# Kernel tuning notes

Hardware: AMD Instinct MI355X
Metric: run time of the kernel (lower is better)

The kernel has to match this reference:

```python
import jax, jax.numpy as jnp
import numpy as np

D_IN = 1024
D_OUT = 1024
NUM_HEADS = 16
HEAD_DIM = D_OUT // NUM_HEADS


def setup_inputs() -> dict:
    key = jax.random.key(0)
    ks = jax.random.split(key, 6)
    s = 0.02
    return {
        "x": jax.random.normal(ks[0], (4, 2048, D_IN), dtype=jnp.float32),
        "Wq": jax.random.normal(ks[1], (D_IN, D_OUT), dtype=jnp.float32) * s,
        "Wk": jax.random.normal(ks[2], (D_IN, D_OUT), dtype=jnp.float32) * s,
        "Wv": jax.random.normal(ks[3], (D_IN, D_OUT), dtype=jnp.float32) * s,
        "Wo": jax.random.normal(ks[4], (D_OUT, D_OUT), dtype=jnp.float32) * s,
        "bo": jax.random.normal(ks[5], (D_OUT,), dtype=jnp.float32) * s,
    }


def reference(x, Wq, Wk, Wv, Wo, bo):
    B, S, _ = x.shape
    # QKV projections (no bias), split into heads: [B, H, S, Dh]
    def split_heads(t):
        return t.reshape(B, S, NUM_HEADS, HEAD_DIM).transpose(0, 2, 1, 3)

    q = split_heads(x @ Wq)
    k = split_heads(x @ Wk)
    v = split_heads(x @ Wv)

    # causal scores [B, H, S, S]; note: original masks BEFORE scaling,
    # but -inf is scale-invariant so softmax(scores/sqrt(d)) with mask is identical.
    scores = jnp.einsum("bhqd,bhkd->bhqk", q, k) / jnp.sqrt(jnp.asarray(HEAD_DIM, x.dtype))
    causal = jnp.tril(jnp.ones((S, S), dtype=bool))
    scores = jnp.where(causal, scores, -jnp.inf)
    attn = jax.nn.softmax(scores, axis=-1)
    # dropout p=0.0 -> identity
    ctx = jnp.einsum("bhqk,bhkd->bhqd", attn, v)  # [B, H, S, Dh]
    ctx = ctx.transpose(0, 2, 1, 3).reshape(B, S, D_OUT)
    return ctx @ Wo + bo
```

## Files before the change

### kernel.cpp

```cpp
#include <hip/hip_runtime.h>
#include <hip/hip_bf16.h>
#include <math.h>


typedef __attribute__((ext_vector_type(8))) short short8;
typedef __attribute__((ext_vector_type(4))) float f32x4;

#define MFMA_BF16(a, b, c) __builtin_amdgcn_mfma_f32_16x16x32_bf16((a), (b), (c), 0, 0, 0)

__device__ __forceinline__ void gld_lds16(const void* g, void* l) {
  __builtin_amdgcn_global_load_lds((const __attribute__((address_space(1))) void*)g,
                                   (__attribute__((address_space(3))) void*)l, 16, 0, 0);
}

__global__ void prep_kernel(const float* __restrict__ x, __hip_bfloat16* __restrict__ xb,
                            const float* __restrict__ W0, const float* __restrict__ W1,
                            const float* __restrict__ W2, const float* __restrict__ W3,
                            __hip_bfloat16* __restrict__ T0, __hip_bfloat16* __restrict__ T1,
                            __hip_bfloat16* __restrict__ T2, __hip_bfloat16* __restrict__ T3) {
  const int bid = blockIdx.x, tid = threadIdx.x;
  if (bid < 8192) {
    int i = bid * 256 + tid;
    float4 v = ((const float4*)x)[i];
    __align__(8) __hip_bfloat16 tmp[4] = {__float2bfloat16(v.x), __float2bfloat16(v.y),
                                          __float2bfloat16(v.z), __float2bfloat16(v.w)};
    ((ushort4*)xb)[i] = *(const ushort4*)tmp;
  } else {
    int zz = bid - 8192;
    int z = zz >> 10, rem = zz & 1023;
    const float* W = (z == 0) ? W0 : (z == 1) ? W1 : (z == 2) ? W2 : W3;
    __hip_bfloat16* Wt = (z == 0) ? T0 : (z == 1) ? T1 : (z == 2) ? T2 : T3;
    __shared__ float tile[32][33];
    int tx = tid & 31, ty = tid >> 5;
    int n0 = (rem & 31) * 32, k0 = (rem >> 5) * 32;
#pragma unroll
    for (int i = 0; i < 4; ++i)
      tile[ty + i * 8][tx] = W[(size_t)(k0 + ty + i * 8) * 1024 + n0 + tx];
    __syncthreads();
#pragma unroll
    for (int i = 0; i < 4; ++i)
      Wt[(size_t)(n0 + ty + i * 8) * 1024 + k0 + tx] = __float2bfloat16(tile[tx][ty + i * 8]);
  }
}

__global__ __launch_bounds__(256, 2) void gemm_qkv(
    const __hip_bfloat16* __restrict__ A, const __hip_bfloat16* __restrict__ Bt,
    __hip_bfloat16* __restrict__ q, __hip_bfloat16* __restrict__ k,
    __hip_bfloat16* __restrict__ vT) {
  __shared__ __align__(16) __hip_bfloat16 As[128 * 64];
  __shared__ __align__(16) __hip_bfloat16 Bs[128 * 64];
  const int tid = threadIdx.x;
  const int lane = tid & 63, wid = tid >> 6;
  const int quad = lane >> 4, l16 = lane & 15;
  const int part = blockIdx.x >> 3;
  const int n0 = (blockIdx.x & 7) * 128;
  const int gn0 = part * 1024 + n0;
  const int m0 = blockIdx.y * 128;
  const int wm = (wid & 1) * 64, wn = (wid >> 1) * 64;
  const int swz = l16 & 7;

  f32x4 acc[4][4] = {};

  for (int k0 = 0; k0 < 1024; k0 += 64) {
    __syncthreads();
#pragma unroll
    for (int i = 0; i < 4; ++i) {
      int sbase = __builtin_amdgcn_readfirstlane(wid * 256 + i * 64);
      int s = sbase + lane;
      int row = s >> 3;
      int ch = (s & 7) ^ (row & 7);
      gld_lds16(A + (size_t)(m0 + row) * 1024 + k0 + ch * 8, &As[sbase * 8]);
      gld_lds16(Bt + (size_t)(gn0 + row) * 1024 + k0 + ch * 8, &Bs[sbase * 8]);
    }
    __syncthreads();

    short8 af[4][2], bfr[4][2];
#pragma unroll
    for (int t = 0; t < 4; ++t)
#pragma unroll
      for (int kc = 0; kc < 2; ++kc) {
        int chp = (kc * 4 + quad) ^ swz;
        af[t][kc]  = *(const short8*)&As[(wm + t * 16 + l16) * 64 + chp * 8];
        bfr[t][kc] = *(const short8*)&Bs[(wn + t * 16 + l16) * 64 + chp * 8];
      }
#pragma unroll
    for (int kc = 0; kc < 2; ++kc)
#pragma unroll
      for (int mt = 0; mt < 4; ++mt)
#pragma unroll
        for (int nt = 0; nt < 4; ++nt)
          acc[mt][nt] = MFMA_BF16(af[mt][kc], bfr[nt][kc], acc[mt][nt]);
  }

  const float CSCL = 0.18033688011112042f;
  if (part < 2) {
    __hip_bfloat16* C = (part == 0) ? q : k;
    const float scl = (part == 0) ? CSCL : 1.0f;
#pragma unroll
    for (int mt = 0; mt < 4; ++mt)
#pragma unroll
      for (int nt = 0; nt < 4; ++nt) {
        int row = m0 + wm + mt * 16 + quad * 4;
        int col = n0 + wn + nt * 16 + l16;
#pragma unroll
        for (int r = 0; r < 4; ++r)
          C[(size_t)(row + r) * 1024 + col] = __float2bfloat16(acc[mt][nt][r] * scl);
      }
  } else {
#pragma unroll
    for (int mt = 0; mt < 4; ++mt)
#pragma unroll
      for (int nt = 0; nt < 4; ++nt) {
        int row = m0 + wm + mt * 16 + quad * 4;
        int nn = n0 + wn + nt * 16 + l16;
        __align__(8) __hip_bfloat16 p4[4];
#pragma unroll
        for (int r = 0; r < 4; ++r) p4[r] = __float2bfloat16(acc[mt][nt][r]);
        *(ushort4*)(vT + (size_t)nn * 8192 + row) = *(const ushort4*)p4;
      }
  }
}

__global__ __launch_bounds__(256, 2) void gemm_bt_f32out(
    const __hip_bfloat16* __restrict__ A, const __hip_bfloat16* __restrict__ Bt,
    float* __restrict__ C, const float* __restrict__ bias, int M, int N, int K) {
  __shared__ __align__(16) __hip_bfloat16 As[128 * 64];
  __shared__ __align__(16) __hip_bfloat16 Bs[128 * 64];
  const int tid = threadIdx.x;
  const int lane = tid & 63, wid = tid >> 6;
  const int quad = lane >> 4, l16 = lane & 15;
  const int m0 = blockIdx.y * 128, n0 = blockIdx.x * 128;
  const int wm = (wid & 1) * 64, wn = (wid >> 1) * 64;
  const int swz = l16 & 7;

  f32x4 acc[4][4] = {};

  for (int k0 = 0; k0 < K; k0 += 64) {
    __syncthreads();
#pragma unroll
    for (int i = 0; i < 4; ++i) {
      int sbase = __builtin_amdgcn_readfirstlane(wid * 256 + i * 64);
      int s = sbase + lane;
      int row = s >> 3;
      int ch = (s & 7) ^ (row & 7);
      gld_lds16(A + (size_t)(m0 + row) * K + k0 + ch * 8, &As[sbase * 8]);
      gld_lds16(Bt + (size_t)(n0 + row) * K + k0 + ch * 8, &Bs[sbase * 8]);
    }
    __syncthreads();

    short8 af[4][2], bfr[4][2];
#pragma unroll
    for (int t = 0; t < 4; ++t)
#pragma unroll
      for (int kc = 0; kc < 2; ++kc) {
        int chp = (kc * 4 + quad) ^ swz;
        af[t][kc]  = *(const short8*)&As[(wm + t * 16 + l16) * 64 + chp * 8];
        bfr[t][kc] = *(const short8*)&Bs[(wn + t * 16 + l16) * 64 + chp * 8];
      }
#pragma unroll
    for (int kc = 0; kc < 2; ++kc)
#pragma unroll
      for (int mt = 0; mt < 4; ++mt)
#pragma unroll
        for (int nt = 0; nt < 4; ++nt)
          acc[mt][nt] = MFMA_BF16(af[mt][kc], bfr[nt][kc], acc[mt][nt]);
  }

#pragma unroll
  for (int mt = 0; mt < 4; ++mt)
#pragma unroll
    for (int nt = 0; nt < 4; ++nt) {
      int row = m0 + wm + mt * 16 + quad * 4;
      int col = n0 + wn + nt * 16 + l16;
      float b = bias[col];
#pragma unroll
      for (int r = 0; r < 4; ++r)
        C[(size_t)(row + r) * N + col] = acc[mt][nt][r] + b;
    }
}

__global__ __launch_bounds__(256, 2) void attn_kernel(
    const __hip_bfloat16* __restrict__ Q, const __hip_bfloat16* __restrict__ Km,
    const __hip_bfloat16* __restrict__ vT, __hip_bfloat16* __restrict__ ctx) {
  const int bid = blockIdx.x;
  const int xcd = bid & 7, loc = bid >> 3;
  const int grp = xcd * 8 + (loc >> 3);
  const int p = loc & 7;
  const int h = grp & 15, b = grp >> 4;
  const size_t rbase = (size_t)b * 2048;
  const int tid = threadIdx.x, lane = tid & 63, wid = tid >> 6;
  const int quad = lane >> 4, l16 = lane & 15;
  const int sw = l16 & 7;

  __shared__ __align__(16) __hip_bfloat16 Ks[2][64 * 64];
  __shared__ __align__(16) __hip_bfloat16 Vs[2][64 * 64];
  __shared__ __align__(16) __hip_bfloat16 Ps[4][32 * 64];

  const float NEG_BIG = -1e30f;

#pragma unroll 1
  for (int sub = 0; sub < 2; ++sub) {
    const int t = sub ? (15 - p) : p;
    const int q0 = t * 128;
    const int qw = q0 + wid * 32;
    const int nkt = 2 * t + 2;

    __syncthreads();
    {
#pragma unroll
      for (int i = 0; i < 2; ++i) {
        int sbase = __builtin_amdgcn_readfirstlane(i * 256 + wid * 64);
        int s = sbase + lane, row = s >> 3, lch = (s & 7) ^ (row & 7);
        gld_lds16(Km + (rbase + row) * 1024 + h * 64 + lch * 8, &Ks[0][sbase * 8]);
        gld_lds16(vT + (size_t)(h * 64 + row) * 8192 + rbase + lch * 8, &Vs[0][sbase * 8]);
      }
    }

    short8 qf[2][2];
#pragma unroll
    for (int mt = 0; mt < 2; ++mt)
#pragma unroll
      for (int kc = 0; kc < 2; ++kc)
        qf[mt][kc] = *(const short8*)(Q + (rbase + qw + mt * 16 + l16) * 1024 +
                                      h * 64 + kc * 32 + quad * 8);

    f32x4 o[2][4] = {};
    float lp[2] = {0.f, 0.f};

#pragma unroll 1
    for (int kt = 0; kt < nkt; ++kt) {
      const int cur = kt & 1;
      const int kbase = kt * 64;
      __syncthreads();
      if (kt + 1 < nkt) {
        const int kb = kbase + 64;
#pragma unroll
        for (int i = 0; i < 2; ++i) {
          int sbase = __builtin_amdgcn_readfirstlane(i * 256 + wid * 64);
          int s = sbase + lane, row = s >> 3, lch = (s & 7) ^ (row & 7);
          gld_lds16(Km + (rbase + kb + row) * 1024 + h * 64 + lch * 8,
                    &Ks[cur ^ 1][sbase * 8]);
          gld_lds16(vT + (size_t)(h * 64 + row) * 8192 + rbase + kb + lch * 8,
                    &Vs[cur ^ 1][sbase * 8]);
        }
      }
      const __hip_bfloat16* Kb = &Ks[cur][0];
      const __hip_bfloat16* Vb = &Vs[cur][0];

      if (kbase <= qw + 31) {
        short8 kf[4][2];
#pragma unroll
        for (int nt = 0; nt < 4; ++nt)
#pragma unroll
          for (int kc = 0; kc < 2; ++kc)
            kf[nt][kc] = *(const short8*)&Kb[(nt * 16 + l16) * 64 +
                                             (((kc * 4 + quad) ^ sw) << 3)];
        f32x4 sv[2][4];
#pragma unroll
        for (int mt = 0; mt < 2; ++mt)
#pragma unroll
          for (int nt = 0; nt < 4; ++nt) {
            f32x4 z = {0.f, 0.f, 0.f, 0.f};
            z = MFMA_BF16(kf[nt][0], qf[mt][0], z);
            z = MFMA_BF16(kf[nt][1], qf[mt][1], z);
            sv[mt][nt] = z;
          }
        if (kbase + 63 > qw) {
#pragma unroll
          for (int mt = 0; mt < 2; ++mt)
#pragma unroll
            for (int nt = 0; nt < 4; ++nt)
#pragma unroll
              for (int r = 0; r < 4; ++r) {
                int kpos = kbase + nt * 16 + quad * 4 + r;
                int qrow = qw + mt * 16 + l16;
                if (kpos > qrow) sv[mt][nt][r] = NEG_BIG;
              }
        }
#pragma unroll
        for (int mt = 0; mt < 2; ++mt)
#pragma unroll
          for (int nt = 0; nt < 4; ++nt) {
            __align__(8) __hip_bfloat16 p4[4];
#pragma unroll
            for (int r = 0; r < 4; ++r) {
              float pv = __builtin_amdgcn_exp2f(sv[mt][nt][r]);
              lp[mt] += pv;
              p4[r] = __float2bfloat16(pv);
            }
            int row = mt * 16 + l16;
            int c16 = (nt * 2 + (quad >> 1)) ^ (row & 7);
            *(ushort4*)&Ps[wid][row * 64 + c16 * 8 + (quad & 1) * 4] =
                *(const ushort4*)p4;
          }
        short8 pa[2][2];
#pragma unroll
        for (int mt = 0; mt < 2; ++mt)
#pragma unroll
          for (int kc = 0; kc < 2; ++kc)
            pa[mt][kc] = *(const short8*)&Ps[wid][(mt * 16 + l16) * 64 +
                                                  (((kc * 4 + quad) ^ sw) << 3)];
        short8 vf[4][2];
#pragma unroll
        for (int dt = 0; dt < 4; ++dt)
#pragma unroll
          for (int kc = 0; kc < 2; ++kc)
            vf[dt][kc] = *(const short8*)&Vb[(dt * 16 + l16) * 64 +
                                             (((kc * 4 + quad) ^ sw) << 3)];
#pragma unroll
        for (int mt = 0; mt < 2; ++mt)
#pragma unroll
          for (int dt = 0; dt < 4; ++dt) {
            o[mt][dt] = MFMA_BF16(pa[mt][0], vf[dt][0], o[mt][dt]);
            o[mt][dt] = MFMA_BF16(pa[mt][1], vf[dt][1], o[mt][dt]);
          }
      }
    }

#pragma unroll
    for (int mt = 0; mt < 2; ++mt) {
      lp[mt] += __shfl_xor(lp[mt], 16, 64);
      lp[mt] += __shfl_xor(lp[mt], 32, 64);
    }
#pragma unroll
    for (int mt = 0; mt < 2; ++mt) {
      float inv[4];
#pragma unroll
      for (int r = 0; r < 4; ++r)
        inv[r] = 1.f / __shfl(lp[mt], quad * 4 + r, 64);
#pragma unroll
      for (int dt = 0; dt < 4; ++dt)
#pragma unroll
        for (int r = 0; r < 4; ++r)
          ctx[(rbase + qw + mt * 16 + quad * 4 + r) * 1024 + h * 64 + dt * 16 + l16] =
              __float2bfloat16(o[mt][dt][r] * inv[r]);
    }
  }
}

extern "C" void kernel_launch(void* const* d_in, const int* in_sizes, int n_in,
                              void* d_out, int out_size, void* d_ws, size_t ws_size,
                              hipStream_t stream) {
  const float* x  = (const float*)d_in[0];
  const float* Wq = (const float*)d_in[1];
  const float* Wk = (const float*)d_in[2];
  const float* Wv = (const float*)d_in[3];
  const float* Wo = (const float*)d_in[4];
  const float* bo = (const float*)d_in[5];
  float* out = (float*)d_out;

  char* ws = (char*)d_ws;
  const size_t MB = 1024ull * 1024ull;
  __hip_bfloat16* q   = (__hip_bfloat16*)(ws);
  __hip_bfloat16* k   = (__hip_bfloat16*)(ws + 16 * MB);
  __hip_bfloat16* vT  = (__hip_bfloat16*)(ws + 32 * MB);
  __hip_bfloat16* woT = (__hip_bfloat16*)(ws + 48 * MB);
  __hip_bfloat16* ctx = q;

  char* outc = (char*)d_out;
  __hip_bfloat16* xb    = (__hip_bfloat16*)(outc);
  __hip_bfloat16* wcatT = (__hip_bfloat16*)(outc + 16 * MB);

  prep_kernel<<<8192 + 4096, 256, 0, stream>>>(
      x, xb, Wq, Wk, Wv, Wo,
      wcatT, wcatT + 1024 * 1024, wcatT + 2048 * 1024, woT);

  gemm_qkv<<<dim3(24, 64), 256, 0, stream>>>(xb, wcatT, q, k, vT);

  attn_kernel<<<512, 256, 0, stream>>>(q, k, vT, ctx);

  gemm_bt_f32out<<<dim3(8, 64), 256, 0, stream>>>(ctx, woT, out, bo, 8192, 1024, 1024);
}
```

Measured before the change: 237.7 us.

## Pipeline GEMM K-loop with triple-buffered LDS and 256x128 tiles using 8 waves

Both bf16 GEMMs (QKV projection and output projection) now share a K-loop with 512-thread blocks computing 256x128 tiles. The loop uses a three-slot LDS ring with direct global-to-LDS loads issued two tiles ahead, and splits each tile's MFMA work into two halves separated by raw s_barriers, explicit vmcnt waits and setprio raises. The aim is to hide global load latency behind MFMA work and improve reuse of B tiles. In exchange it uses much more LDS per block (144 KB), which may limit occupancy, and correctness now depends on hand-placed barrier and waitcnt ordering.

```diff
diff --git a/kernel.cpp b/kernel.cpp
--- a/kernel.cpp
+++ b/kernel.cpp
@@ -7,6 +7,10 @@
 typedef __attribute__((ext_vector_type(4))) float f32x4;
 
 #define MFMA_BF16(a, b, c) __builtin_amdgcn_mfma_f32_16x16x32_bf16((a), (b), (c), 0, 0, 0)
+
+#define SBAR() asm volatile("s_barrier" ::: "memory")
+#define VMCNT6() asm volatile("s_waitcnt vmcnt(6)" ::: "memory")
+#define VMCNT0() asm volatile("s_waitcnt vmcnt(0)" ::: "memory")
 
 __device__ __forceinline__ void gld_lds16(const void* g, void* l) {
   __builtin_amdgcn_global_load_lds((const __attribute__((address_space(1))) void*)g,
@@ -43,54 +47,117 @@
   }
 }
 
-__global__ __launch_bounds__(256, 2) void gemm_qkv(
+__device__ __forceinline__ void gemm8p_kloop(
+    const __hip_bfloat16* __restrict__ A, const __hip_bfloat16* __restrict__ Bt,
+    int m0, int gn0, __hip_bfloat16* As_, __hip_bfloat16* Bs_,
+    f32x4 (&acc)[4][4]) {
+  const int tid = threadIdx.x;
+  const int lane = tid & 63, wid = tid >> 6;
+  const int quad = lane >> 4, l16 = lane & 15;
+  const int wm = (wid >> 1) * 64, wn = (wid & 1) * 64;
+  const int sw = l16 & 7;
+
+  auto stage_half = [&](int t, int half, int slot) {
+#pragma unroll
+    for (int li = 0; li < 2; ++li) {
+      int sbase = __builtin_amdgcn_readfirstlane((half * 2 + li) * 512 + wid * 64);
+      int s = sbase + lane, row = s >> 3, ch = (s & 7) ^ (row & 7);
+      gld_lds16(A + (size_t)(m0 + row) * 1024 + t * 64 + ch * 8,
+                As_ + slot * 16384 + sbase * 8);
+    }
+    {
+      int sbase = __builtin_amdgcn_readfirstlane(half * 512 + wid * 64);
+      int s = sbase + lane, row = s >> 3, ch = (s & 7) ^ (row & 7);
+      gld_lds16(Bt + (size_t)(gn0 + row) * 1024 + t * 64 + ch * 8,
+                Bs_ + slot * 8192 + sbase * 8);
+    }
+  };
+
+  auto tile_step = [&](int t, int cur, int st, int mode) {
+    const __hip_bfloat16* Asl = As_ + cur * 16384;
+    const __hip_bfloat16* Bsl = Bs_ + cur * 8192;
+    short8 af[4][2], bf01[2][2], bf23[2][2];
+#pragma unroll
+    for (int mt = 0; mt < 4; ++mt)
+#pragma unroll
+      for (int kc = 0; kc < 2; ++kc)
+        af[mt][kc] = *(const short8*)&Asl[(wm + mt * 16 + l16) * 64 +
+                                          (((kc * 4 + quad) ^ sw) << 3)];
+#pragma unroll
+    for (int nt = 0; nt < 2; ++nt)
+#pragma unroll
+      for (int kc = 0; kc < 2; ++kc)
+        bf01[nt][kc] = *(const short8*)&Bsl[(wn + nt * 16 + l16) * 64 +
+                                            (((kc * 4 + quad) ^ sw) << 3)];
+    if (mode == 0) stage_half(t + 2, 0, st);
+    if (mode != 2) SBAR();
+    __builtin_amdgcn_s_setprio(1);
+#pragma unroll
+    for (int kc = 0; kc < 2; ++kc)
+#pragma unroll
+      for (int mt = 0; mt < 4; ++mt)
+#pragma unroll
+        for (int nt = 0; nt < 2; ++nt)
+          acc[mt][nt] = MFMA_BF16(af[mt][kc], bf01[nt][kc], acc[mt][nt]);
+    __builtin_amdgcn_s_setprio(0);
+    if (mode != 2) SBAR();
+#pragma unroll
+    for (int nt = 0; nt < 2; ++nt)
+#pragma unroll
+      for (int kc = 0; kc < 2; ++kc)
+        bf23[nt][kc] = *(const short8*)&Bsl[(wn + (2 + nt) * 16 + l16) * 64 +
+                                            (((kc * 4 + quad) ^ sw) << 3)];
+    if (mode == 0) stage_half(t + 2, 1, st);
+    if (mode != 2) SBAR();
+    __builtin_amdgcn_s_setprio(1);
+#pragma unroll
+    for (int kc = 0; kc < 2; ++kc)
+#pragma unroll
+      for (int mt = 0; mt < 4; ++mt)
+#pragma unroll
+        for (int nt = 0; nt < 2; ++nt)
+          acc[mt][2 + nt] = MFMA_BF16(af[mt][kc], bf23[nt][kc], acc[mt][2 + nt]);
+    __builtin_amdgcn_s_setprio(0);
+    if (mode == 0) VMCNT6();
+    if (mode == 1) VMCNT0();
+    if (mode != 2) SBAR();
+  };
+
+#pragma unroll
+  for (int h = 0; h < 2; ++h) stage_half(0, h, 0);
+#pragma unroll
+  for (int h = 0; h < 2; ++h) stage_half(1, h, 1);
+  VMCNT6();
+  SBAR();
+
+  int cur = 0, st = 2;
+#pragma unroll 1
+  for (int t = 0; t < 14; ++t) {
+    tile_step(t, cur, st, 0);
+    cur = (cur == 2) ? 0 : cur + 1;
+    st = (st == 2) ? 0 : st + 1;
+  }
+  tile_step(14, 2, 0, 1);
+  tile_step(15, 0, 0, 2);
+}
+
+__global__ __launch_bounds__(512, 2) void gemm_qkv(
     const __hip_bfloat16* __restrict__ A, const __hip_bfloat16* __restrict__ Bt,
     __hip_bfloat16* __restrict__ q, __hip_bfloat16* __restrict__ k,
     __hip_bfloat16* __restrict__ vT) {
-  __shared__ __align__(16) __hip_bfloat16 As[128 * 64];
-  __shared__ __align__(16) __hip_bfloat16 Bs[128 * 64];
+  __shared__ __align__(16) __hip_bfloat16 As[3 * 256 * 64];
+  __shared__ __align__(16) __hip_bfloat16 Bs[3 * 128 * 64];
   const int tid = threadIdx.x;
   const int lane = tid & 63, wid = tid >> 6;
   const int quad = lane >> 4, l16 = lane & 15;
   const int part = blockIdx.x >> 3;
-  const int n0 = (blockIdx.x & 7) * 128;
-  const int gn0 = part * 1024 + n0;
-  const int m0 = blockIdx.y * 128;
-  const int wm = (wid & 1) * 64, wn = (wid >> 1) * 64;
-  const int swz = l16 & 7;
+  const int n0l = (blockIdx.x & 7) * 128;
+  const int gn0 = part * 1024 + n0l;
+  const int m0 = blockIdx.y * 256;
+  const int wm = (wid >> 1) * 64, wn = (wid & 1) * 64;
 
   f32x4 acc[4][4] = {};
-
-  for (int k0 = 0; k0 < 1024; k0 += 64) {
-    __syncthreads();
-#pragma unroll
-    for (int i = 0; i < 4; ++i) {
-      int sbase = __builtin_amdgcn_readfirstlane(wid * 256 + i * 64);
-      int s = sbase + lane;
-      int row = s >> 3;
-      int ch = (s & 7) ^ (row & 7);
-      gld_lds16(A + (size_t)(m0 + row) * 1024 + k0 + ch * 8, &As[sbase * 8]);
-      gld_lds16(Bt + (size_t)(gn0 + row) * 1024 + k0 + ch * 8, &Bs[sbase * 8]);
-    }
-    __syncthreads();
-
-    short8 af[4][2], bfr[4][2];
-#pragma unroll
-    for (int t = 0; t < 4; ++t)
-#pragma unroll
-      for (int kc = 0; kc < 2; ++kc) {
-        int chp = (kc * 4 + quad) ^ swz;
-        af[t][kc]  = *(const short8*)&As[(wm + t * 16 + l16) * 64 + chp * 8];
-        bfr[t][kc] = *(const short8*)&Bs[(wn + t * 16 + l16) * 64 + chp * 8];
-      }
-#pragma unroll
-    for (int kc = 0; kc < 2; ++kc)
-#pragma unroll
-      for (int mt = 0; mt < 4; ++mt)
-#pragma unroll
-        for (int nt = 0; nt < 4; ++nt)
-          acc[mt][nt] = MFMA_BF16(af[mt][kc], bfr[nt][kc], acc[mt][nt]);
-  }
+  gemm8p_kloop(A, Bt, m0, gn0, As, Bs, acc);
 
   const float CSCL = 0.18033688011112042f;
   if (part < 2) {
@@ -101,7 +168,7 @@
 #pragma unroll
       for (int nt = 0; nt < 4; ++nt) {
         int row = m0 + wm + mt * 16 + quad * 4;
-        int col = n0 + wn + nt * 16 + l16;
+        int col = n0l + wn + nt * 16 + l16;
 #pragma unroll
         for (int r = 0; r < 4; ++r)
           C[(size_t)(row + r) * 1024 + col] = __float2bfloat16(acc[mt][nt][r] * scl);
@@ -112,7 +179,7 @@
 #pragma unroll
       for (int nt = 0; nt < 4; ++nt) {
         int row = m0 + wm + mt * 16 + quad * 4;
-        int nn = n0 + wn + nt * 16 + l16;
+        int nn = n0l + wn + nt * 16 + l16;
         __align__(8) __hip_bfloat16 p4[4];
 #pragma unroll
         for (int r = 0; r < 4; ++r) p4[r] = __float2bfloat16(acc[mt][nt][r]);
@@ -121,50 +188,19 @@
   }
 }
 
-__global__ __launch_bounds__(256, 2) void gemm_bt_f32out(
+__global__ __launch_bounds__(512, 2) void gemm_bt_f32out(
     const __hip_bfloat16* __restrict__ A, const __hip_bfloat16* __restrict__ Bt,
-    float* __restrict__ C, const float* __restrict__ bias, int M, int N, int K) {
-  __shared__ __align__(16) __hip_bfloat16 As[128 * 64];
-  __shared__ __align__(16) __hip_bfloat16 Bs[128 * 64];
+    float* __restrict__ C, const float* __restrict__ bias) {
+  __shared__ __align__(16) __hip_bfloat16 As[3 * 256 * 64];
+  __shared__ __align__(16) __hip_bfloat16 Bs[3 * 128 * 64];
   const int tid = threadIdx.x;
   const int lane = tid & 63, wid = tid >> 6;
   const int quad = lane >> 4, l16 = lane & 15;
-  const int m0 = blockIdx.y * 128, n0 = blockIdx.x * 128;
-  const int wm = (wid & 1) * 64, wn = (wid >> 1) * 64;
-  const int swz = l16 & 7;
+  const int n0 = blockIdx.x * 128, m0 = blockIdx.y * 256;
+  const int wm = (wid >> 1) * 64, wn = (wid & 1) * 64;
 
   f32x4 acc[4][4] = {};
-
-  for (int k0 = 0; k0 < K; k0 += 64) {
-    __syncthreads();
-#pragma unroll
-    for (int i = 0; i < 4; ++i) {
-      int sbase = __builtin_amdgcn_readfirstlane(wid * 256 + i * 64);
-      int s = sbase + lane;
-      int row = s >> 3;
-      int ch = (s & 7) ^ (row & 7);
-      gld_lds16(A + (size_t)(m0 + row) * K + k0 + ch * 8, &As[sbase * 8]);
-      gld_lds16(Bt + (size_t)(n0 + row) * K + k0 + ch * 8, &Bs[sbase * 8]);
-    }
-    __syncthreads();
-
-    short8 af[4][2], bfr[4][2];
-#pragma unroll
-    for (int t = 0; t < 4; ++t)
-#pragma unroll
-      for (int kc = 0; kc < 2; ++kc) {
-        int chp = (kc * 4 + quad) ^ swz;
-        af[t][kc]  = *(const short8*)&As[(wm + t * 16 + l16) * 64 + chp * 8];
-        bfr[t][kc] = *(const short8*)&Bs[(wn + t * 16 + l16) * 64 + chp * 8];
-      }
-#pragma unroll
-    for (int kc = 0; kc < 2; ++kc)
-#pragma unroll
-      for (int mt = 0; mt < 4; ++mt)
-#pragma unroll
-        for (int nt = 0; nt < 4; ++nt)
-          acc[mt][nt] = MFMA_BF16(af[mt][kc], bfr[nt][kc], acc[mt][nt]);
-  }
+  gemm8p_kloop(A, Bt, m0, n0, As, Bs, acc);
 
 #pragma unroll
   for (int mt = 0; mt < 4; ++mt)
@@ -175,7 +211,7 @@
       float b = bias[col];
 #pragma unroll
       for (int r = 0; r < 4; ++r)
-        C[(size_t)(row + r) * N + col] = acc[mt][nt][r] + b;
+        C[(size_t)(row + r) * 1024 + col] = acc[mt][nt][r] + b;
     }
 }
 
@@ -365,9 +401,9 @@
       x, xb, Wq, Wk, Wv, Wo,
       wcatT, wcatT + 1024 * 1024, wcatT + 2048 * 1024, woT);
 
-  gemm_qkv<<<dim3(24, 64), 256, 0, stream>>>(xb, wcatT, q, k, vT);
+  gemm_qkv<<<dim3(24, 32), 512, 0, stream>>>(xb, wcatT, q, k, vT);
 
   attn_kernel<<<512, 256, 0, stream>>>(q, k, vT, ctx);
 
-  gemm_bt_f32out<<<dim3(8, 64), 256, 0, stream>>>(ctx, woT, out, bo, 8192, 1024, 1024);
-}
+  gemm_bt_f32out<<<dim3(8, 32), 512, 0, stream>>>(ctx, woT, out, bo);
+}
```

Result: faster. 233.0 us (-2.0%).

## Rewrite QKV GEMM with 256x256 tiles, 8 waves, double-buffered LDS pipeline

Applied to the files above, without the earlier changes.

The QKV projection GEMM moves from 128x128 tiles with 4 waves to 256x256 tiles with 8 waves. LDS is double-buffered, so loads for the next k-step are issued mid-iteration. The MFMA work is split into four phases separated by explicit s_barrier/vmcnt waits and s_setprio, overlapping global->LDS copies with compute and raising arithmetic intensity per block. The costs are a larger LDS footprint (128KB per block), more registers per wave, and only 384 blocks, which may leave the 256 CUs unevenly loaded.

```diff
diff --git a/kernel.cpp b/kernel.cpp
--- a/kernel.cpp
+++ b/kernel.cpp
@@ -7,6 +7,10 @@
 typedef __attribute__((ext_vector_type(4))) float f32x4;
 
 #define MFMA_BF16(a, b, c) __builtin_amdgcn_mfma_f32_16x16x32_bf16((a), (b), (c), 0, 0, 0)
+
+#define SBAR() asm volatile("s_barrier" ::: "memory")
+#define VMCNT4() asm volatile("s_waitcnt vmcnt(4)" ::: "memory")
+#define VMCNT0() asm volatile("s_waitcnt vmcnt(0)" ::: "memory")
 
 __device__ __forceinline__ void gld_lds16(const void* g, void* l) {
   __builtin_amdgcn_global_load_lds((const __attribute__((address_space(1))) void*)g,
@@ -43,53 +47,129 @@
   }
 }
 
-__global__ __launch_bounds__(256, 2) void gemm_qkv(
+__global__ __launch_bounds__(512, 2) void gemm_qkv(
     const __hip_bfloat16* __restrict__ A, const __hip_bfloat16* __restrict__ Bt,
     __hip_bfloat16* __restrict__ q, __hip_bfloat16* __restrict__ k,
     __hip_bfloat16* __restrict__ vT) {
-  __shared__ __align__(16) __hip_bfloat16 As[128 * 64];
-  __shared__ __align__(16) __hip_bfloat16 Bs[128 * 64];
+  __shared__ __align__(16) __hip_bfloat16 LA[2][256 * 64];
+  __shared__ __align__(16) __hip_bfloat16 LB[2][256 * 64];
   const int tid = threadIdx.x;
   const int lane = tid & 63, wid = tid >> 6;
   const int quad = lane >> 4, l16 = lane & 15;
-  const int part = blockIdx.x >> 3;
-  const int n0 = (blockIdx.x & 7) * 128;
-  const int gn0 = part * 1024 + n0;
-  const int m0 = blockIdx.y * 128;
-  const int wm = (wid & 1) * 64, wn = (wid >> 1) * 64;
-  const int swz = l16 & 7;
-
-  f32x4 acc[4][4] = {};
-
-  for (int k0 = 0; k0 < 1024; k0 += 64) {
-    __syncthreads();
-#pragma unroll
-    for (int i = 0; i < 4; ++i) {
-      int sbase = __builtin_amdgcn_readfirstlane(wid * 256 + i * 64);
-      int s = sbase + lane;
-      int row = s >> 3;
-      int ch = (s & 7) ^ (row & 7);
-      gld_lds16(A + (size_t)(m0 + row) * 1024 + k0 + ch * 8, &As[sbase * 8]);
-      gld_lds16(Bt + (size_t)(gn0 + row) * 1024 + k0 + ch * 8, &Bs[sbase * 8]);
-    }
-    __syncthreads();
-
-    short8 af[4][2], bfr[4][2];
-#pragma unroll
-    for (int t = 0; t < 4; ++t)
-#pragma unroll
-      for (int kc = 0; kc < 2; ++kc) {
-        int chp = (kc * 4 + quad) ^ swz;
-        af[t][kc]  = *(const short8*)&As[(wm + t * 16 + l16) * 64 + chp * 8];
-        bfr[t][kc] = *(const short8*)&Bs[(wn + t * 16 + l16) * 64 + chp * 8];
-      }
+  const int part = blockIdx.x >> 2;
+  const int n0l = (blockIdx.x & 3) * 256;
+  const int gn0 = part * 1024 + n0l;
+  const int m0 = blockIdx.y * 256;
+  const int wm = (wid >> 2) * 128, wn = (wid & 3) * 64;
+  const int sw = l16 & 7;
+
+  auto stage = [&](const __hip_bfloat16* G, int g0, int t, __hip_bfloat16* Ld, int h) {
+#pragma unroll
+    for (int li = 0; li < 2; ++li) {
+      int sbase = __builtin_amdgcn_readfirstlane(h * 1024 + li * 512 + wid * 64);
+      int s = sbase + lane, row = s >> 3, ch = (s & 7) ^ (row & 7);
+      gld_lds16(G + (size_t)(g0 + row) * 1024 + t * 64 + ch * 8, Ld + sbase * 8);
+    }
+  };
+
+  f32x4 acc[8][4] = {};
+
+  stage(A, m0, 0, &LA[0][0], 0);
+  stage(A, m0, 0, &LA[0][0], 1);
+  stage(Bt, gn0, 0, &LB[0][0], 0);
+  stage(Bt, gn0, 0, &LB[0][0], 1);
+  stage(Bt, gn0, 1, &LB[1][0], 0);
+  stage(Bt, gn0, 1, &LB[1][0], 1);
+  VMCNT4();
+  SBAR();
+
+#pragma unroll 1
+  for (int t = 0; t < 16; ++t) {
+    const int b = t & 1;
+    const __hip_bfloat16* LAb = &LA[b][0];
+    const __hip_bfloat16* LBb = &LB[b][0];
+    const bool sync = (t < 15);
+    short8 af[8][2], bf01[2][2], bf23[2][2];
+
+#pragma unroll
+    for (int mt = 0; mt < 4; ++mt)
+#pragma unroll
+      for (int kc = 0; kc < 2; ++kc)
+        af[mt][kc] = *(const short8*)&LAb[(wm + mt * 16 + l16) * 64 +
+                                          (((kc * 4 + quad) ^ sw) << 3)];
+#pragma unroll
+    for (int nt = 0; nt < 2; ++nt)
+#pragma unroll
+      for (int kc = 0; kc < 2; ++kc)
+        bf01[nt][kc] = *(const short8*)&LBb[(wn + nt * 16 + l16) * 64 +
+                                            (((kc * 4 + quad) ^ sw) << 3)];
+    if (t + 1 < 16) stage(A, m0, t + 1, &LA[b ^ 1][0], 0);
+    if (sync) SBAR();
+    __builtin_amdgcn_s_setprio(1);
 #pragma unroll
     for (int kc = 0; kc < 2; ++kc)
 #pragma unroll
       for (int mt = 0; mt < 4; ++mt)
 #pragma unroll
-        for (int nt = 0; nt < 4; ++nt)
-          acc[mt][nt] = MFMA_BF16(af[mt][kc], bfr[nt][kc], acc[mt][nt]);
+        for (int nt = 0; nt < 2; ++nt)
+          acc[mt][nt] = MFMA_BF16(af[mt][kc], bf01[nt][kc], acc[mt][nt]);
+    __builtin_amdgcn_s_setprio(0);
+    if (sync) SBAR();
+
+#pragma unroll
+    for (int mt = 4; mt < 8; ++mt)
+#pragma unroll
+      for (int kc = 0; kc < 2; ++kc)
+        af[mt][kc] = *(const short8*)&LAb[(wm + mt * 16 + l16) * 64 +
+                                          (((kc * 4 + quad) ^ sw) << 3)];
+    if (t + 1 < 16) stage(A, m0, t + 1, &LA[b ^ 1][0], 1);
+    if (sync) SBAR();
+    __builtin_amdgcn_s_setprio(1);
+#pragma unroll
+    for (int kc = 0; kc < 2; ++kc)
+#pragma unroll
+      for (int mt = 4; mt < 8; ++mt)
+#pragma unroll
+        for (int nt = 0; nt < 2; ++nt)
+          acc[mt][nt] = MFMA_BF16(af[mt][kc], bf01[nt][kc], acc[mt][nt]);
+    __builtin_amdgcn_s_setprio(0);
+    if (sync) SBAR();
+
+#pragma unroll
+    for (int nt = 0; nt < 2; ++nt)
+#pragma unroll
+      for (int kc = 0; kc < 2; ++kc)
+        bf23[nt][kc] = *(const short8*)&LBb[(wn + (2 + nt) * 16 + l16) * 64 +
+                                            (((kc * 4 + quad) ^ sw) << 3)];
+    if (sync) SBAR();
+    __builtin_amdgcn_s_setprio(1);
+#pragma unroll
+    for (int kc = 0; kc < 2; ++kc)
+#pragma unroll
+      for (int mt = 4; mt < 8; ++mt)
+#pragma unroll
+        for (int nt = 0; nt < 2; ++nt)
+          acc[mt][2 + nt] = MFMA_BF16(af[mt][kc], bf23[nt][kc], acc[mt][2 + nt]);
+    __builtin_amdgcn_s_setprio(0);
+    if (sync) SBAR();
+
+    if (t + 2 < 16) {
+      stage(Bt, gn0, t + 2, &LB[b][0], 0);
+      stage(Bt, gn0, t + 2, &LB[b][0], 1);
+    }
+    if (sync) SBAR();
+    __builtin_amdgcn_s_setprio(1);
+#pragma unroll
+    for (int kc = 0; kc < 2; ++kc)
+#pragma unroll
+      for (int mt = 0; mt < 4; ++mt)
+#pragma unroll
+        for (int nt = 0; nt < 2; ++nt)
+          acc[mt][2 + nt] = MFMA_BF16(af[mt][kc], bf23[nt][kc], acc[mt][2 + nt]);
+    __builtin_amdgcn_s_setprio(0);
+    if (t < 14) VMCNT4();
+    else if (t == 14) VMCNT0();
+    if (sync) SBAR();
   }
 
   const float CSCL = 0.18033688011112042f;
@@ -97,22 +177,22 @@
     __hip_bfloat16* C = (part == 0) ? q : k;
     const float scl = (part == 0) ? CSCL : 1.0f;
 #pragma unroll
-    for (int mt = 0; mt < 4; ++mt)
+    for (int mt = 0; mt < 8; ++mt)
 #pragma unroll
       for (int nt = 0; nt < 4; ++nt) {
         int row = m0 + wm + mt * 16 + quad * 4;
-        int col = n0 + wn + nt * 16 + l16;
+        int col = n0l + wn + nt * 16 + l16;
 #pragma unroll
         for (int r = 0; r < 4; ++r)
           C[(size_t)(row + r) * 1024 + col] = __float2bfloat16(acc[mt][nt][r] * scl);
       }
   } else {
 #pragma unroll
-    for (int mt = 0; mt < 4; ++mt)
+    for (int mt = 0; mt < 8; ++mt)
 #pragma unroll
       for (int nt = 0; nt < 4; ++nt) {
         int row = m0 + wm + mt * 16 + quad * 4;
-        int nn = n0 + wn + nt * 16 + l16;
+        int nn = n0l + wn + nt * 16 + l16;
         __align__(8) __hip_bfloat16 p4[4];
 #pragma unroll
         for (int r = 0; r < 4; ++r) p4[r] = __float2bfloat16(acc[mt][nt][r]);
@@ -365,7 +445,7 @@
       x, xb, Wq, Wk, Wv, Wo,
       wcatT, wcatT + 1024 * 1024, wcatT + 2048 * 1024, woT);
 
-  gemm_qkv<<<dim3(24, 64), 256, 0, stream>>>(xb, wcatT, q, k, vT);
+  gemm_qkv<<<dim3(12, 32), 512, 0, stream>>>(xb, wcatT, q, k, vT);
 
   attn_kernel<<<512, 256, 0, stream>>>(q, k, vT, ctx);
 
```

Result: slower. 250.0 us (+5.2%).
